# Performance work log

Hardware: AMD Instinct MI355X
Metric: run time of the kernel (lower is better)

The kernel has to match this reference:

```python
import jax, jax.numpy as jnp
import numpy as np

IN_DIM, OUT_DIM, NUM, K = 256, 128, 16, 3
BATCH = 2048
MONO = ((0, 1), (1, -1))  # (input dim index, direction)


def _make_grid():
    # linspace over grid_range, then extend k knots on each side with uniform step h
    lo, hi = -1.0, 1.0
    h = (hi - lo) / NUM
    pts = np.linspace(lo, hi, NUM + 1)
    ext = np.concatenate([lo + h * np.arange(-K, 0), pts, hi + h * np.arange(1, K + 1)])
    return jnp.asarray(np.tile(ext, (IN_DIM, 1)), dtype=jnp.float32)  # (in_dim, num+2k+1)


def _b_batch(x, grid, k):
    # de-Boor B-spline basis. x: (B, in), grid: (in, G). Returns (B, in, G-k-1).
    xg = x[:, :, None]
    g = grid[None, :, :]
    B = ((xg >= g[:, :, :-1]) & (xg < g[:, :, 1:])).astype(x.dtype)
    for p in range(1, k + 1):
        left = (xg - g[:, :, :-(p + 1)]) / (g[:, :, p:-1] - g[:, :, :-(p + 1)]) * B[:, :, :-1]
        right = (g[:, :, p + 1:] - xg) / (g[:, :, p + 1:] - g[:, :, 1:-p]) * B[:, :, 1:]
        B = left + right
    return B


def setup_inputs() -> dict:
    key = jax.random.key(0)
    k1, k2, k3, k4 = jax.random.split(key, 4)
    inv_sqrt_in = 1.0 / np.sqrt(IN_DIM)
    x = 0.4 * jax.random.normal(k1, (BATCH, IN_DIM), dtype=jnp.float32)
    coef = 0.1 * jax.random.normal(k2, (IN_DIM, OUT_DIM, NUM + K), dtype=jnp.float32)
    scale_sp_raw = jnp.ones((IN_DIM, OUT_DIM), dtype=jnp.float32) * inv_sqrt_in
    scale_base = (jax.random.uniform(k3, (IN_DIM, OUT_DIM), dtype=jnp.float32) * 2.0 - 1.0) * inv_sqrt_in
    grid = _make_grid()
    mask = jnp.ones((IN_DIM, OUT_DIM), dtype=jnp.float32)
    base_mask = jnp.ones((IN_DIM, OUT_DIM), dtype=jnp.float32)
    for dim, _ in MONO:
        base_mask = base_mask.at[dim, :].set(0.0)
    return {"x": x, "coef": coef, "scale_sp_raw": scale_sp_raw, "scale_base": scale_base,
            "grid": grid, "mask": mask, "base_mask": base_mask}


def reference(x, coef, scale_sp_raw, scale_base, grid, mask, base_mask):
    bs = x.shape[0]
    preacts = jnp.broadcast_to(x[:, None, :], (bs, OUT_DIM, IN_DIM))
    # monotonic reparameterization: softplus + cumsum over spline-coefficient axis
    for dim, direction in MONO:
        delta = jnp.cumsum(jax.nn.softplus(coef[dim]), axis=-1)  # (out, num+k)
        coef = coef.at[dim].set(direction * delta)
    # coef2curve: basis (B, in, num+k) contracted with coef (in, out, num+k)
    basis = _b_batch(x, grid, K)
    y = jnp.einsum('bid,iod->bio', basis, coef)  # (B, in, out)
    postspline = jnp.transpose(y, (0, 2, 1))
    scale_sp = jax.nn.softplus(scale_sp_raw)
    y = scale_sp[None, :, :] * y
    base = base_mask * scale_base[None, :, :] * jax.nn.silu(x)[:, :, None]
    y = y + base
    y = mask[None, :, :] * y
    postacts = jnp.transpose(y, (0, 2, 1))
    out = jnp.sum(y, axis=1)  # (B, out)
    return out, preacts, postacts, postspline
```

## Files before the change

### kernel.cpp

```cpp
#include <hip/hip_runtime.h>
#include <math.h>

#define IN_DIM   256
#define OUT_DIM  128
#define NCOEF    19
#define BATCH    2048
#define BT       4
#define TILE_F   (IN_DIM * NCOEF)

__device__ __forceinline__ float softplus_f(float v) {
  return (v > 20.0f) ? v : log1pf(expf(v));
}

__device__ __forceinline__ void load_lds16(const float* g, float* l) {
  __builtin_amdgcn_global_load_lds(
      (const __attribute__((address_space(1))) void*)g,
      (__attribute__((address_space(3))) void*)l,
      16, 0, 0);
}

__global__ void kan_prep(const float* __restrict__ coef,
                         const float* __restrict__ ssp,
                         const float* __restrict__ sbase,
                         const float* __restrict__ mask,
                         const float* __restrict__ bmask,
                         float* __restrict__ coefT,
                         float* __restrict__ At,
                         float* __restrict__ Bt) {
  int g = blockIdx.x * 256 + threadIdx.x;
  int o = g >> 8;
  int i = g & 255;
  const float* src = coef + ((size_t)i * OUT_DIM + o) * NCOEF;
  float c[NCOEF];
#pragma unroll
  for (int d = 0; d < NCOEF; ++d) c[d] = src[d];
  if (i < 2) {
    float dir = (i == 0) ? 1.0f : -1.0f;
    float acc = 0.0f;
#pragma unroll
    for (int d = 0; d < NCOEF; ++d) { acc += softplus_f(c[d]); c[d] = dir * acc; }
  }
  float* dst = coefT + (size_t)g * NCOEF;
#pragma unroll
  for (int d = 0; d < NCOEF; ++d) dst[d] = c[d];
  int io = i * OUT_DIM + o;
  float m = mask[io];
  At[g] = m * softplus_f(ssp[io]);
  Bt[g] = m * bmask[io] * sbase[io];
}

__device__ __forceinline__ float wave_reduce(float v) {
  int t;
  t = __builtin_amdgcn_update_dpp(0, __float_as_int(v), 0x111, 0xf, 0xf, true); v += __int_as_float(t);
  t = __builtin_amdgcn_update_dpp(0, __float_as_int(v), 0x112, 0xf, 0xf, true); v += __int_as_float(t);
  t = __builtin_amdgcn_update_dpp(0, __float_as_int(v), 0x114, 0xf, 0xf, true); v += __int_as_float(t);
  t = __builtin_amdgcn_update_dpp(0, __float_as_int(v), 0x118, 0xf, 0xf, true); v += __int_as_float(t);
  t = __builtin_amdgcn_update_dpp(0, __float_as_int(v), 0x142, 0xa, 0xf, true); v += __int_as_float(t);
  t = __builtin_amdgcn_update_dpp(0, __float_as_int(v), 0x143, 0xc, 0xf, true); v += __int_as_float(t);
  return v;
}

__global__ __launch_bounds__(512, 6) void kan_main(
    const float* __restrict__ x,
    const float* __restrict__ coefT,
    const float* __restrict__ At,
    const float* __restrict__ Bt,
    float* __restrict__ out,
    float* __restrict__ preacts,
    float* __restrict__ postacts,
    float* __restrict__ postspline) {
  __shared__ __align__(16) float s_coef[2][TILE_F];
  __shared__ float s_out[BT][OUT_DIM][4];

  const int tid  = threadIdx.x;
  const int i    = tid & 255;
  const int bsub = tid >> 8;
  const int wq   = (tid >> 6) & 3;
  const int b0   = blockIdx.x * BT;

  float xv[2], sl[2], wv[2][4];
  int   wi[2][4];

#pragma unroll
  for (int bb = 0; bb < 2; ++bb) {
    int b = b0 + bsub * 2 + bb;
    float xx = x[(size_t)b * IN_DIM + i];
    xv[bb] = xx;
    sl[bb] = xx / (1.0f + expf(-xx));

    float tpos = (xx + 1.375f) * 8.0f;
    int j = (int)floorf(tpos);
    bool valid = (j >= 0) && (j <= 21);
    int jc = valid ? j : 3;

    float N[4] = {1.0f, 0.0f, 0.0f, 0.0f};
#pragma unroll
    for (int p = 1; p <= 3; ++p) {
      const float inv = (p == 1) ? 8.0f : ((p == 2) ? 4.0f : (8.0f / 3.0f));
      float Np[4] = {0.0f, 0.0f, 0.0f, 0.0f};
#pragma unroll
      for (int m = 0; m < 4; ++m) {
        if (m <= p) {
          float ga = -1.375f + 0.125f * (float)(jc + m - p);
          float v = 0.0f;
          if (m > 0) v += (xx - ga) * inv * N[m - 1];
          if (m < p) v += ((ga + 0.125f * (float)(p + 1)) - xx) * inv * N[m];
          Np[m] = v;
        }
      }
#pragma unroll
      for (int m = 0; m < 4; ++m) N[m] = Np[m];
    }
#pragma unroll
    for (int r = 0; r < 4; ++r) {
      int dr = jc - 3 + r;
      bool ok = valid && (dr >= 0) && (dr <= 18);
      wv[bb][r] = ok ? N[r] : 0.0f;
      wi[bb][r] = i * NCOEF + (ok ? dr : 0);
    }
  }

  {
    const float* src = coefT;
    float* dst = &s_coef[0][0];
    load_lds16(src + tid * 4,        dst + tid * 4);
    load_lds16(src + 2048 + tid * 4, dst + 2048 + tid * 4);
    if (tid < 192) load_lds16(src + 4096 + tid * 4, dst + 4096 + tid * 4);
  }
  float a_cur = At[i];
  float b_cur = Bt[i];
  __syncthreads();

  size_t off0 = ((size_t)(b0 + bsub * 2)     * OUT_DIM) * IN_DIM + i;
  size_t off1 = ((size_t)(b0 + bsub * 2 + 1) * OUT_DIM) * IN_DIM + i;

#pragma unroll 2
  for (int o = 0; o < OUT_DIM; ++o) {
    const int cur = o & 1;
    const float* sc = &s_coef[cur][0];

    if (o + 1 < OUT_DIM) {
      const float* src = coefT + (size_t)(o + 1) * TILE_F;
      float* dst = &s_coef[cur ^ 1][0];
      load_lds16(src + tid * 4,        dst + tid * 4);
      load_lds16(src + 2048 + tid * 4, dst + 2048 + tid * 4);
      if (tid < 192) load_lds16(src + 4096 + tid * 4, dst + 4096 + tid * 4);
    }
    asm volatile("" ::: "memory");

    float a_nxt = 0.0f, b_nxt = 0.0f;
    if (o + 1 < OUT_DIM) {
      a_nxt = At[(o + 1) * IN_DIM + i];
      b_nxt = Bt[(o + 1) * IN_DIM + i];
    }

#pragma unroll
    for (int bb = 0; bb < 2; ++bb) {
      int bl = bsub * 2 + bb;
      float sp = wv[bb][0] * sc[wi[bb][0]]
               + wv[bb][1] * sc[wi[bb][1]]
               + wv[bb][2] * sc[wi[bb][2]]
               + wv[bb][3] * sc[wi[bb][3]];
      float ya = a_cur * sp + b_cur * sl[bb];

      size_t off = (bb == 0 ? off0 : off1) + (size_t)o * IN_DIM;
      __builtin_nontemporal_store(sp,     postspline + off);
      __builtin_nontemporal_store(ya,     postacts   + off);
      __builtin_nontemporal_store(xv[bb], preacts    + off);

      float red = wave_reduce(ya);
      if ((tid & 63) == 63) s_out[bl][o][wq] = red;
    }

    asm volatile("s_waitcnt vmcnt(6)" ::: "memory");
    __builtin_amdgcn_s_barrier();

    a_cur = a_nxt;
    b_cur = b_nxt;
  }

  __syncthreads();
  {
    int bl = tid >> 7;
    int o  = tid & 127;
    float s = s_out[bl][o][0] + s_out[bl][o][1] + s_out[bl][o][2] + s_out[bl][o][3];
    out[(size_t)(b0 + bl) * OUT_DIM + o] = s;
  }
}

extern "C" void kernel_launch(void* const* d_in, const int* in_sizes, int n_in,
                              void* d_out, int out_size, void* d_ws, size_t ws_size,
                              hipStream_t stream) {
  (void)in_sizes; (void)n_in; (void)out_size; (void)ws_size;

  const float* x     = (const float*)d_in[0];
  const float* coef  = (const float*)d_in[1];
  const float* ssp   = (const float*)d_in[2];
  const float* sbase = (const float*)d_in[3];
  const float* mask  = (const float*)d_in[5];
  const float* bmask = (const float*)d_in[6];

  float* coefT = (float*)d_ws;
  float* At    = coefT + (size_t)OUT_DIM * IN_DIM * NCOEF;
  float* Bt    = At + (size_t)OUT_DIM * IN_DIM;

  float* out        = (float*)d_out;
  float* preacts    = out + (size_t)BATCH * OUT_DIM;
  float* postacts   = preacts + (size_t)BATCH * OUT_DIM * IN_DIM;
  float* postspline = postacts + (size_t)BATCH * OUT_DIM * IN_DIM;

  kan_prep<<<(OUT_DIM * IN_DIM) / 256, 256, 0, stream>>>(coef, ssp, sbase, mask, bmask,
                                                         coefT, At, Bt);
  kan_main<<<BATCH / BT, 512, 0, stream>>>(x, coefT, At, Bt,
                                           out, preacts, postacts, postspline);
}
```

Measured before the change: 175.5 us.

## Triple-buffer coefficient tiles in LDS with two-ahead prefetch

```diff
diff --git a/kernel.cpp b/kernel.cpp
--- a/kernel.cpp
+++ b/kernel.cpp
@@ -17,6 +17,12 @@
       (const __attribute__((address_space(1))) void*)g,
       (__attribute__((address_space(3))) void*)l,
       16, 0, 0);
+}
+
+__device__ __forceinline__ void stage_tile(const float* src, float* dst, int tid) {
+  load_lds16(src + tid * 4,        dst + tid * 4);
+  load_lds16(src + 2048 + tid * 4, dst + 2048 + tid * 4);
+  if (tid < 192) load_lds16(src + 4096 + tid * 4, dst + 4096 + tid * 4);
 }
 
 __global__ void kan_prep(const float* __restrict__ coef,
@@ -60,7 +66,7 @@
   return v;
 }
 
-__global__ __launch_bounds__(512, 6) void kan_main(
+__global__ __launch_bounds__(512, 4) void kan_main(
     const float* __restrict__ x,
     const float* __restrict__ coefT,
     const float* __restrict__ At,
@@ -69,7 +75,7 @@
     float* __restrict__ preacts,
     float* __restrict__ postacts,
     float* __restrict__ postspline) {
-  __shared__ __align__(16) float s_coef[2][TILE_F];
+  __shared__ __align__(16) float s_coef[3][TILE_F];
   __shared__ float s_out[BT][OUT_DIM][4];
 
   const int tid  = threadIdx.x;
@@ -120,63 +126,50 @@
     }
   }
 
-  {
-    const float* src = coefT;
-    float* dst = &s_coef[0][0];
-    load_lds16(src + tid * 4,        dst + tid * 4);
-    load_lds16(src + 2048 + tid * 4, dst + 2048 + tid * 4);
-    if (tid < 192) load_lds16(src + 4096 + tid * 4, dst + 4096 + tid * 4);
-  }
-  float a_cur = At[i];
-  float b_cur = Bt[i];
+  stage_tile(coefT,          &s_coef[0][0], tid);
+  stage_tile(coefT + TILE_F, &s_coef[1][0], tid);
+  float a_cur = At[i],             b_cur = Bt[i];
+  float a_nx1 = At[IN_DIM + i],    b_nx1 = Bt[IN_DIM + i];
   __syncthreads();
 
   size_t off0 = ((size_t)(b0 + bsub * 2)     * OUT_DIM) * IN_DIM + i;
   size_t off1 = ((size_t)(b0 + bsub * 2 + 1) * OUT_DIM) * IN_DIM + i;
 
-#pragma unroll 2
+#pragma unroll 3
   for (int o = 0; o < OUT_DIM; ++o) {
-    const int cur = o & 1;
-    const float* sc = &s_coef[cur][0];
-
-    if (o + 1 < OUT_DIM) {
-      const float* src = coefT + (size_t)(o + 1) * TILE_F;
-      float* dst = &s_coef[cur ^ 1][0];
-      load_lds16(src + tid * 4,        dst + tid * 4);
-      load_lds16(src + 2048 + tid * 4, dst + 2048 + tid * 4);
-      if (tid < 192) load_lds16(src + 4096 + tid * 4, dst + 4096 + tid * 4);
+    const float* sc = &s_coef[o % 3][0];
+
+    {
+      const int on = (o + 2 < OUT_DIM) ? o + 2 : OUT_DIM - 1;
+      stage_tile(coefT + (size_t)on * TILE_F, &s_coef[(o + 2) % 3][0], tid);
+      asm volatile("" ::: "memory");
+      float a_nx2 = At[on * IN_DIM + i];
+      float b_nx2 = Bt[on * IN_DIM + i];
+
+#pragma unroll
+      for (int bb = 0; bb < 2; ++bb) {
+        int bl = bsub * 2 + bb;
+        float sp = wv[bb][0] * sc[wi[bb][0]]
+                 + wv[bb][1] * sc[wi[bb][1]]
+                 + wv[bb][2] * sc[wi[bb][2]]
+                 + wv[bb][3] * sc[wi[bb][3]];
+        float ya = a_cur * sp + b_cur * sl[bb];
+
+        size_t off = (bb == 0 ? off0 : off1) + (size_t)o * IN_DIM;
+        __builtin_nontemporal_store(sp,     postspline + off);
+        __builtin_nontemporal_store(ya,     postacts   + off);
+        __builtin_nontemporal_store(xv[bb], preacts    + off);
+
+        float red = wave_reduce(ya);
+        if ((tid & 63) == 63) s_out[bl][o][wq] = red;
+      }
+
+      asm volatile("s_waitcnt vmcnt(11)" ::: "memory");
+      __builtin_amdgcn_s_barrier();
+
+      a_cur = a_nx1; b_cur = b_nx1;
+      a_nx1 = a_nx2; b_nx1 = b_nx2;
     }
-    asm volatile("" ::: "memory");
-
-    float a_nxt = 0.0f, b_nxt = 0.0f;
-    if (o + 1 < OUT_DIM) {
-      a_nxt = At[(o + 1) * IN_DIM + i];
-      b_nxt = Bt[(o + 1) * IN_DIM + i];
-    }
-
-#pragma unroll
-    for (int bb = 0; bb < 2; ++bb) {
-      int bl = bsub * 2 + bb;
-      float sp = wv[bb][0] * sc[wi[bb][0]]
-               + wv[bb][1] * sc[wi[bb][1]]
-               + wv[bb][2] * sc[wi[bb][2]]
-               + wv[bb][3] * sc[wi[bb][3]];
-      float ya = a_cur * sp + b_cur * sl[bb];
-
-      size_t off = (bb == 0 ? off0 : off1) + (size_t)o * IN_DIM;
-      __builtin_nontemporal_store(sp,     postspline + off);
-      __builtin_nontemporal_store(ya,     postacts   + off);
-      __builtin_nontemporal_store(xv[bb], preacts    + off);
-
-      float red = wave_reduce(ya);
-      if ((tid & 63) == 63) s_out[bl][o][wq] = red;
-    }
-
-    asm volatile("s_waitcnt vmcnt(6)" ::: "memory");
-    __builtin_amdgcn_s_barrier();
-
-    a_cur = a_nxt;
-    b_cur = b_nxt;
   }
 
   __syncthreads();
```

After: 207.0 us. 1.18x slower.
